# Kernel optimization log

Measured on AMD Instinct MI355X. Metric: run time of the kernel, lower is better.

## Reference

```python
import jax, jax.numpy as jnp
import numpy as np

B, S, DIN, DH, NB = 4, 2048, 256, 128, 50
LN_EPS = 1e-5
THRESHOLDS = (0.5, 1.0, 2.0, 4.0)


def _layernorm(x, g, b):
    m = jnp.mean(x, axis=-1, keepdims=True)
    v = jnp.mean((x - m) ** 2, axis=-1, keepdims=True)
    return (x - m) * jax.lax.rsqrt(v + LN_EPS) * g + b


def setup_inputs() -> dict:
    key = jax.random.key(0)
    ks = jax.random.split(key, 12)
    single_repr = jax.random.normal(ks[0], (B, S, DIN), jnp.float32)
    # coordinates spread out so the <=15A local neighborhood is nontrivial
    coordinates = jax.random.normal(ks[1], (B, S, 3), jnp.float32) * 12.0
    mask = jnp.ones((B, S), jnp.float32)
    sc = 0.05
    return {
        'single_repr': single_repr,
        'coordinates': coordinates,
        'mask': mask,
        'W1': jax.random.normal(ks[2], (DIN, DH), jnp.float32) * sc,
        'b1': jnp.zeros((DH,), jnp.float32),
        'g1': jnp.ones((DH,), jnp.float32),
        'be1': jnp.zeros((DH,), jnp.float32),
        'W2': jax.random.normal(ks[3], (DH, DH), jnp.float32) * sc,
        'b2': jnp.zeros((DH,), jnp.float32),
        'g2': jnp.ones((DH,), jnp.float32),
        'be2': jnp.zeros((DH,), jnp.float32),
        'W3': jax.random.normal(ks[4], (DH, NB), jnp.float32) * sc,
        'b3': jnp.zeros((NB,), jnp.float32),
        'temperature': jnp.ones((1,), jnp.float32),
    }


def reference(single_repr, coordinates, mask, W1, b1, g1, be1, W2, b2, g2, be2, W3, b3, temperature):
    # ---- confidence MLP (dropout in eval mode = identity) ----
    h = jax.nn.relu(_layernorm(single_repr @ W1 + b1, g1, be1))
    h = jax.nn.relu(_layernorm(h @ W2 + b2, g2, be2))
    logits = (h @ W3 + b3) / temperature          # [B, S, NB]
    probs = jax.nn.softmax(logits, axis=-1)

    # ---- vectorized pLDDT (replaces the per-residue Python loop) ----
    diff = coordinates[:, :, None, :] - coordinates[:, None, :, :]   # [B,S,S,3]
    D = jnp.sqrt(jnp.sum(diff * diff, axis=-1))                      # [B,S,S]
    maskb = mask > 0.0
    local = (D <= 15.0) & maskb[:, :, None] & maskb[:, None, :]      # [B,S,S]
    counts = jnp.sum(local, axis=-1).astype(jnp.float32)             # [B,S]
    frac_sum = jnp.zeros((B, S), jnp.float32)
    for t in THRESHOLDS:  # fixed small loop over 4 thresholds
        within = jnp.sum((D <= t) & local, axis=-1).astype(jnp.float32)
        frac_sum = frac_sum + within / jnp.maximum(counts, 1.0)
    plddt = jnp.where(counts > 0, frac_sum / len(THRESHOLDS) * 100.0, 0.0)

    # ---- final masking, as in torch forward ----
    plddt = plddt * mask
    logits_m = logits * mask[:, :, None]
    probs_m = probs * mask[:, :, None]
    return plddt, logits_m, probs_m
```

## Files before the change

kernel.cpp:

```cpp
#include <hip/hip_runtime.h>
#include <float.h>
#include <math.h>

#define B_   4
#define S_   2048
#define DIN_ 256
#define DH_  128
#define NB_  50
#define NBP_ 64
#define ROWS (B_ * S_)
#define MB   16

#define SETUP_BLOCKS 14
#define PLDDT_ROWSPB 32
#define PLDDT_BLOCKS (ROWS / PLDDT_ROWSPB)
#define MLP_BLOCKS   (ROWS / MB)

typedef __attribute__((ext_vector_type(8))) short  short8;
typedef __attribute__((ext_vector_type(4))) float  f32x4;
typedef __attribute__((ext_vector_type(2))) float  f32x2;

__device__ __forceinline__ unsigned short bf16_rne(float f) {
    unsigned u = __builtin_bit_cast(unsigned, f);
    u = u + 0x7fffu + ((u >> 16) & 1u);
    return (unsigned short)(u >> 16);
}

__global__ __launch_bounds__(512) void setup_w(
    const float* __restrict__ W1, const float* __restrict__ W2,
    const float* __restrict__ W3, unsigned short* __restrict__ wt)
{
    const int t = blockIdx.x * 512 + threadIdx.x;
    const int l = t & 63, m = l & 15, kg = l >> 4;
    float src[8];
    int dst;
    if (t < 4096) {
        const int c = t >> 6, nt = c >> 3, ks = c & 7;
        const int n = nt * 16 + m, k = ks * 32 + kg * 8;
#pragma unroll
        for (int i = 0; i < 8; ++i) src[i] = W1[(k + i) * DH_ + n];
        dst = t * 8;
    } else if (t < 6144) {
        const int s = t - 4096, c = s >> 6, nt = c >> 2, ks = c & 3;
        const int n = nt * 16 + m, k = ks * 32 + kg * 8;
#pragma unroll
        for (int i = 0; i < 8; ++i) src[i] = W2[(k + i) * DH_ + n];
        dst = 32768 + s * 8;
    } else {
        const int s = t - 6144, c = s >> 6, nt = c >> 2, ks = c & 3;
        const int n = nt * 16 + m, k = ks * 32 + kg * 8;
#pragma unroll
        for (int i = 0; i < 8; ++i) src[i] = (n < NB_) ? W3[(k + i) * NB_ + n] : 0.f;
        dst = 49152 + s * 8;
    }
    union { short8 v; unsigned short u[8]; } H;
#pragma unroll
    for (int i = 0; i < 8; ++i) H.u[i] = bf16_rne(src[i]);
    *(short8*)&wt[dst] = H.v;
}

union SharedU {
    struct {
        unsigned short sA[MB * DIN_];
        float sStats[MB][20];
        float sL[MB * NBP_];
    } mlp;
    f32x4 sP[S_];
};

__global__ __launch_bounds__(512) void fused_kernel(
    const float* __restrict__ x, const float* __restrict__ coords,
    const float* __restrict__ mask,
    const float* __restrict__ b1, const float* __restrict__ g1, const float* __restrict__ be1,
    const float* __restrict__ b2, const float* __restrict__ g2, const float* __restrict__ be2,
    const float* __restrict__ b3, const float* __restrict__ temp,
    const unsigned short* __restrict__ wt,
    float* __restrict__ out_plddt,
    float* __restrict__ out_logits, float* __restrict__ out_probs)
{
    __shared__ SharedU sh;
    const int tid  = threadIdx.x;
    const int lane = tid & 63;
    const int w    = tid >> 6;

    if (blockIdx.x < PLDDT_BLOCKS) {
        const int pb   = blockIdx.x;
        const int row0 = pb * PLDDT_ROWSPB;
        const int b    = row0 >> 11;
        const int ib0  = row0 & (S_ - 1);

        const float* cb = coords + (size_t)b * S_ * 3;
        const float* mb = mask   + (size_t)b * S_;

        {
            union { f32x4 v[3]; float f[12]; } C;
            const float* cp = cb + tid * 12;
#pragma unroll
            for (int q = 0; q < 3; ++q) C.v[q] = *(const f32x4*)(cp + q * 4);
            union { f32x4 v; float f[4]; } M;
            M.v = *(const f32x4*)(mb + tid * 4);
#pragma unroll
            for (int q = 0; q < 4; ++q)
                sh.sP[tid * 4 + q] = (f32x4){C.f[q*3], C.f[q*3+1], C.f[q*3+2], M.f[q]};
        }
        __syncthreads();

        f32x4 PI[4];
#pragma unroll
        for (int ii = 0; ii < 4; ++ii) PI[ii] = sh.sP[ib0 + w * 4 + ii];

        const f32x2 Px[2] = {{PI[0][0], PI[1][0]}, {PI[2][0], PI[3][0]}};
        const f32x2 Py[2] = {{PI[0][1], PI[1][1]}, {PI[2][1], PI[3][1]}};
        const f32x2 Pz[2] = {{PI[0][2], PI[1][2]}, {PI[2][2], PI[3][2]}};

        int cnt[4] = {0,0,0,0}, ws[4] = {0,0,0,0};
#pragma unroll 2
        for (int j = lane; j < S_; j += 64) {
            const f32x4 p = sh.sP[j];
            const float gd = (p[3] > 0.f) ? 1e-35f : 1e30f;
            const f32x2 pg = {gd, gd};
            const f32x2 px = {p[0], p[0]}, py = {p[1], p[1]}, pz = {p[2], p[2]};
#pragma unroll
            for (int pr = 0; pr < 2; ++pr) {
                f32x2 dx = Px[pr] - px;
                f32x2 dy = Py[pr] - py;
                f32x2 dz = Pz[pr] - pz;
                f32x2 d2 = __builtin_elementwise_fma(dx, dx,
                           __builtin_elementwise_fma(dy, dy,
                           __builtin_elementwise_fma(dz, dz, pg)));
#pragma unroll
                for (int el = 0; el < 2; ++el) {
                    const int ii = pr * 2 + el;
                    const float d2e = d2[el];
                    cnt[ii] += (d2e <= 225.f);
                    const unsigned u = __builtin_bit_cast(unsigned, d2e);
                    int c = (132 - (int)((u - 1u) >> 23)) >> 1;
                    c = c < 0 ? 0 : (c > 4 ? 4 : c);
                    ws[ii] += c;
                }
            }
        }
#pragma unroll
        for (int ii = 0; ii < 4; ++ii) {
            int acc = (cnt[ii] << 16) | ws[ii];
            for (int off = 32; off; off >>= 1) acc += __shfl_xor(acc, off);
            if (lane == 0) {
                const int ct = acc >> 16, wv = acc & 0xFFFF;
                const float r = (ct > 0) ? (wv * 25.f / (float)ct) : 0.f;
                out_plddt[row0 + w * 4 + ii] = r * PI[ii][3];
            }
        }
    } else {
        unsigned short* sA = sh.mlp.sA;
        const int m    = lane & 15;
        const int kg   = lane >> 4;
        const int row0 = (blockIdx.x - PLDDT_BLOCKS) * MB;

        {
            const int r  = tid >> 5;
            const int kc = (tid & 31) << 3;
            const float* xp = x + (size_t)(row0 + r) * DIN_ + kc;
            f32x4 a = *(const f32x4*)xp;
            f32x4 b = *(const f32x4*)(xp + 4);
            union { short8 v; unsigned short u[8]; } H;
#pragma unroll
            for (int i = 0; i < 8; ++i)
                H.u[i] = bf16_rne((i < 4) ? a[i] : b[i - 4]);
            const int idx = (r * 256 + kc) ^ ((r & 7) << 3);
            *(short8*)&sA[idx] = H.v;
        }
        __syncthreads();

        const int n12 = w * 16 + m;

        f32x4 aA = {0,0,0,0}, aB = {0,0,0,0};
        {
            const unsigned short* bp = wt + (w * 8) * 512;
#pragma unroll
            for (int ks = 0; ks < 8; ++ks) {
                const int ia = (m * 256 + ks * 32 + kg * 8) ^ ((m & 7) << 3);
                short8 ah = *(const short8*)&sA[ia];
                short8 bh = *(const short8*)&bp[ks * 512 + lane * 8];
                f32x4& ac = (ks & 1) ? aB : aA;
                ac = __builtin_amdgcn_mfma_f32_16x16x32_bf16(ah, bh, ac, 0, 0, 0);
            }
        }

        {
            const float bb = b1[n12], gg = g1[n12], ee = be1[n12];
            float v[4];
#pragma unroll
            for (int j = 0; j < 4; ++j) v[j] = aA[j] + aB[j] + bb;
#pragma unroll
            for (int j = 0; j < 4; ++j) {
                float sv = v[j], qv = v[j] * v[j];
                for (int off = 1; off < 16; off <<= 1) { sv += __shfl_xor(sv, off); qv += __shfl_xor(qv, off); }
                if (m == 0) { sh.mlp.sStats[kg * 4 + j][w * 2] = sv; sh.mlp.sStats[kg * 4 + j][w * 2 + 1] = qv; }
            }
            __syncthreads();
#pragma unroll
            for (int j = 0; j < 4; ++j) {
                const int r = kg * 4 + j;
                f32x4 s0 = *(const f32x4*)&sh.mlp.sStats[r][0];
                f32x4 s1 = *(const f32x4*)&sh.mlp.sStats[r][4];
                f32x4 s2 = *(const f32x4*)&sh.mlp.sStats[r][8];
                f32x4 s3 = *(const f32x4*)&sh.mlp.sStats[r][12];
                const float S = s0[0]+s0[2]+s1[0]+s1[2]+s2[0]+s2[2]+s3[0]+s3[2];
                const float Q = s0[1]+s0[3]+s1[1]+s1[3]+s2[1]+s2[3]+s3[1]+s3[3];
                const float mean = S * (1.f / DH_);
                const float inv  = rsqrtf(Q * (1.f / DH_) - mean * mean + 1e-5f);
                const float h = fmaxf(fmaf((v[j] - mean) * inv, gg, ee), 0.f);
                const int idx = (r * 128 + n12) ^ ((r & 7) << 3);
                sA[idx] = bf16_rne(h);
            }
        }
        __syncthreads();

        aA = (f32x4){0,0,0,0}; aB = (f32x4){0,0,0,0};
        {
            const unsigned short* bp = wt + 32768 + (w * 4) * 512;
#pragma unroll
            for (int ks = 0; ks < 4; ++ks) {
                const int ia = (m * 128 + ks * 32 + kg * 8) ^ ((m & 7) << 3);
                short8 ah = *(const short8*)&sA[ia];
                short8 bh = *(const short8*)&bp[ks * 512 + lane * 8];
                f32x4& ac = (ks & 1) ? aB : aA;
                ac = __builtin_amdgcn_mfma_f32_16x16x32_bf16(ah, bh, ac, 0, 0, 0);
            }
        }

        {
            const float bb = b2[n12], gg = g2[n12], ee = be2[n12];
            float v[4];
#pragma unroll
            for (int j = 0; j < 4; ++j) v[j] = aA[j] + aB[j] + bb;
#pragma unroll
            for (int j = 0; j < 4; ++j) {
                float sv = v[j], qv = v[j] * v[j];
                for (int off = 1; off < 16; off <<= 1) { sv += __shfl_xor(sv, off); qv += __shfl_xor(qv, off); }
                if (m == 0) { sh.mlp.sStats[kg * 4 + j][w * 2] = sv; sh.mlp.sStats[kg * 4 + j][w * 2 + 1] = qv; }
            }
            __syncthreads();
#pragma unroll
            for (int j = 0; j < 4; ++j) {
                const int r = kg * 4 + j;
                f32x4 s0 = *(const f32x4*)&sh.mlp.sStats[r][0];
                f32x4 s1 = *(const f32x4*)&sh.mlp.sStats[r][4];
                f32x4 s2 = *(const f32x4*)&sh.mlp.sStats[r][8];
                f32x4 s3 = *(const f32x4*)&sh.mlp.sStats[r][12];
                const float S = s0[0]+s0[2]+s1[0]+s1[2]+s2[0]+s2[2]+s3[0]+s3[2];
                const float Q = s0[1]+s0[3]+s1[1]+s1[3]+s2[1]+s2[3]+s3[1]+s3[3];
                const float mean = S * (1.f / DH_);
                const float inv  = rsqrtf(Q * (1.f / DH_) - mean * mean + 1e-5f);
                const float h = fmaxf(fmaf((v[j] - mean) * inv, gg, ee), 0.f);
                const int idx = (r * 128 + n12) ^ ((r & 7) << 3);
                sA[idx] = bf16_rne(h);
            }
        }
        __syncthreads();

        if (w < 4) {
            f32x4 cA = {0,0,0,0}, cB = {0,0,0,0};
            const unsigned short* bp = wt + 49152 + (w * 4) * 512;
#pragma unroll
            for (int ks = 0; ks < 4; ++ks) {
                const int ia = (m * 128 + ks * 32 + kg * 8) ^ ((m & 7) << 3);
                short8 ah = *(const short8*)&sA[ia];
                short8 bh = *(const short8*)&bp[ks * 512 + lane * 8];
                f32x4& ac = (ks & 1) ? cB : cA;
                ac = __builtin_amdgcn_mfma_f32_16x16x32_bf16(ah, bh, ac, 0, 0, 0);
            }
            const int n = w * 16 + m;
            const float bv = (n < NB_) ? b3[n] : 0.f;
            const float invT = 1.f / temp[0];
#pragma unroll
            for (int j = 0; j < 4; ++j)
                sh.mlp.sL[(kg * 4 + j) * NBP_ + n] = (cA[j] + cB[j] + bv) * invT;
        }
        __syncthreads();

        if (tid < 256) {
            const int r  = tid >> 4;
            const int c0 = (tid & 15) * 4;
            f32x4 lg = *(const f32x4*)&sh.mlp.sL[r * NBP_ + c0];
            float mx = -FLT_MAX;
#pragma unroll
            for (int i = 0; i < 4; ++i) if (c0 + i < NB_) mx = fmaxf(mx, lg[i]);
            for (int off = 1; off < 16; off <<= 1) mx = fmaxf(mx, __shfl_xor(mx, off));
            float e[4]; float sm = 0.f;
#pragma unroll
            for (int i = 0; i < 4; ++i) { e[i] = (c0 + i < NB_) ? expf(lg[i] - mx) : 0.f; sm += e[i]; }
            for (int off = 1; off < 16; off <<= 1) sm += __shfl_xor(sm, off);
            const float isum = 1.f / sm;
            const float mk = mask[row0 + r];
            float* ol = out_logits + (size_t)(row0 + r) * NB_;
            float* op = out_probs  + (size_t)(row0 + r) * NB_;
#pragma unroll
            for (int i = 0; i < 4; ++i) {
                const int c = c0 + i;
                if (c < NB_) { ol[c] = lg[i] * mk; op[c] = e[i] * isum * mk; }
            }
        }
    }
}

extern "C" void kernel_launch(void* const* d_in, const int* in_sizes, int n_in,
                              void* d_out, int out_size, void* d_ws, size_t ws_size,
                              hipStream_t stream) {
    const float* x      = (const float*)d_in[0];
    const float* coords = (const float*)d_in[1];
    const float* mask   = (const float*)d_in[2];
    const float* W1  = (const float*)d_in[3];
    const float* b1  = (const float*)d_in[4];
    const float* g1  = (const float*)d_in[5];
    const float* be1 = (const float*)d_in[6];
    const float* W2  = (const float*)d_in[7];
    const float* b2  = (const float*)d_in[8];
    const float* g2  = (const float*)d_in[9];
    const float* be2 = (const float*)d_in[10];
    const float* W3  = (const float*)d_in[11];
    const float* b3  = (const float*)d_in[12];
    const float* temp= (const float*)d_in[13];

    float* out        = (float*)d_out;
    float* out_plddt  = out;
    float* out_logits = out + (size_t)ROWS;
    float* out_probs  = out_logits + (size_t)ROWS * NB_;

    unsigned short* wt = (unsigned short*)d_ws;

    setup_w<<<SETUP_BLOCKS, 512, 0, stream>>>(W1, W2, W3, wt);
    fused_kernel<<<PLDDT_BLOCKS + MLP_BLOCKS, 512, 0, stream>>>(
        x, coords, mask, b1, g1, be1, b2, g2, be2, b3, temp, wt,
        out_plddt, out_logits, out_probs);
}
```

Measured before the change: 24.15 us.

## Interleave pLDDT and MLP blocks and halve rows per pLDDT block

pLDDT blocks now handle 16 rows instead of 32, so each wave computes 2 rows. Even block indices do pLDDT work and odd ones do MLP, so the two workloads are mixed across the grid instead of running one after the other. Each pLDDT block still stages all 2048 coordinates into shared memory, and there are now twice as many such blocks, which doubles that staging traffic. The count and weight sums are packed into a single accumulator per row, removing some arithmetic and shuffle work.

```diff
diff --git a/kernel.cpp b/kernel.cpp
--- a/kernel.cpp
+++ b/kernel.cpp
@@ -12,8 +12,8 @@
 #define MB   16
 
 #define SETUP_BLOCKS 14
-#define PLDDT_ROWSPB 32
-#define PLDDT_BLOCKS (ROWS / PLDDT_ROWSPB)
+#define PL_ROWS      16
+#define PL_BLOCKS    (ROWS / PL_ROWS)
 #define MLP_BLOCKS   (ROWS / MB)
 
 typedef __attribute__((ext_vector_type(8))) short  short8;
@@ -83,9 +83,9 @@
     const int lane = tid & 63;
     const int w    = tid >> 6;
 
-    if (blockIdx.x < PLDDT_BLOCKS) {
-        const int pb   = blockIdx.x;
-        const int row0 = pb * PLDDT_ROWSPB;
+    if ((blockIdx.x & 1) == 0) {
+        const int pb   = blockIdx.x >> 1;
+        const int row0 = pb * PL_ROWS;
         const int b    = row0 >> 11;
         const int ib0  = row0 & (S_ - 1);
 
@@ -105,56 +105,61 @@
         }
         __syncthreads();
 
-        f32x4 PI[4];
-#pragma unroll
-        for (int ii = 0; ii < 4; ++ii) PI[ii] = sh.sP[ib0 + w * 4 + ii];
-
-        const f32x2 Px[2] = {{PI[0][0], PI[1][0]}, {PI[2][0], PI[3][0]}};
-        const f32x2 Py[2] = {{PI[0][1], PI[1][1]}, {PI[2][1], PI[3][1]}};
-        const f32x2 Pz[2] = {{PI[0][2], PI[1][2]}, {PI[2][2], PI[3][2]}};
-
-        int cnt[4] = {0,0,0,0}, ws[4] = {0,0,0,0};
-#pragma unroll 2
+        const f32x4 PI0 = sh.sP[ib0 + w * 2 + 0];
+        const f32x4 PI1 = sh.sP[ib0 + w * 2 + 1];
+        const f32x2 Px = {PI0[0], PI1[0]};
+        const f32x2 Py = {PI0[1], PI1[1]};
+        const f32x2 Pz = {PI0[2], PI1[2]};
+
+        int acc0 = 0, acc1 = 0;
+#pragma unroll 4
         for (int j = lane; j < S_; j += 64) {
             const f32x4 p = sh.sP[j];
             const float gd = (p[3] > 0.f) ? 1e-35f : 1e30f;
             const f32x2 pg = {gd, gd};
             const f32x2 px = {p[0], p[0]}, py = {p[1], p[1]}, pz = {p[2], p[2]};
-#pragma unroll
-            for (int pr = 0; pr < 2; ++pr) {
-                f32x2 dx = Px[pr] - px;
-                f32x2 dy = Py[pr] - py;
-                f32x2 dz = Pz[pr] - pz;
-                f32x2 d2 = __builtin_elementwise_fma(dx, dx,
-                           __builtin_elementwise_fma(dy, dy,
-                           __builtin_elementwise_fma(dz, dz, pg)));
-#pragma unroll
-                for (int el = 0; el < 2; ++el) {
-                    const int ii = pr * 2 + el;
-                    const float d2e = d2[el];
-                    cnt[ii] += (d2e <= 225.f);
-                    const unsigned u = __builtin_bit_cast(unsigned, d2e);
-                    int c = (132 - (int)((u - 1u) >> 23)) >> 1;
-                    c = c < 0 ? 0 : (c > 4 ? 4 : c);
-                    ws[ii] += c;
-                }
-            }
-        }
-#pragma unroll
-        for (int ii = 0; ii < 4; ++ii) {
-            int acc = (cnt[ii] << 16) | ws[ii];
-            for (int off = 32; off; off >>= 1) acc += __shfl_xor(acc, off);
-            if (lane == 0) {
-                const int ct = acc >> 16, wv = acc & 0xFFFF;
+            f32x2 dx = Px - px;
+            f32x2 dy = Py - py;
+            f32x2 dz = Pz - pz;
+            f32x2 d2 = __builtin_elementwise_fma(dx, dx,
+                       __builtin_elementwise_fma(dy, dy,
+                       __builtin_elementwise_fma(dz, dz, pg)));
+            {
+                const float d2e = d2[0];
+                const unsigned u = __builtin_bit_cast(unsigned, d2e);
+                int c = (132 - (int)((u - 1u) >> 23)) >> 1;
+                c = c < 0 ? 0 : (c > 4 ? 4 : c);
+                acc0 += c + ((d2e <= 225.f) ? 65536 : 0);
+            }
+            {
+                const float d2e = d2[1];
+                const unsigned u = __builtin_bit_cast(unsigned, d2e);
+                int c = (132 - (int)((u - 1u) >> 23)) >> 1;
+                c = c < 0 ? 0 : (c > 4 ? 4 : c);
+                acc1 += c + ((d2e <= 225.f) ? 65536 : 0);
+            }
+        }
+        for (int off = 32; off; off >>= 1) {
+            acc0 += __shfl_xor(acc0, off);
+            acc1 += __shfl_xor(acc1, off);
+        }
+        if (lane == 0) {
+            {
+                const int ct = acc0 >> 16, wv = acc0 & 0xFFFF;
                 const float r = (ct > 0) ? (wv * 25.f / (float)ct) : 0.f;
-                out_plddt[row0 + w * 4 + ii] = r * PI[ii][3];
+                out_plddt[row0 + w * 2 + 0] = r * PI0[3];
+            }
+            {
+                const int ct = acc1 >> 16, wv = acc1 & 0xFFFF;
+                const float r = (ct > 0) ? (wv * 25.f / (float)ct) : 0.f;
+                out_plddt[row0 + w * 2 + 1] = r * PI1[3];
             }
         }
     } else {
         unsigned short* sA = sh.mlp.sA;
         const int m    = lane & 15;
         const int kg   = lane >> 4;
-        const int row0 = (blockIdx.x - PLDDT_BLOCKS) * MB;
+        const int row0 = (blockIdx.x >> 1) * MB;
 
         {
             const int r  = tid >> 5;
@@ -330,7 +335,7 @@
     unsigned short* wt = (unsigned short*)d_ws;
 
     setup_w<<<SETUP_BLOCKS, 512, 0, stream>>>(W1, W2, W3, wt);
-    fused_kernel<<<PLDDT_BLOCKS + MLP_BLOCKS, 512, 0, stream>>>(
+    fused_kernel<<<PL_BLOCKS + MLP_BLOCKS, 512, 0, stream>>>(
         x, coords, mask, b1, g1, be1, b2, g2, be2, b3, temp, wt,
         out_plddt, out_logits, out_probs);
 }
```

Result: slower. 25.92 us (+7.3%).
